# Kernel tuning notes

Measured on AMD Instinct MI355X. Metric: run time of the kernel, lower is better.

The kernel has to match this reference:

```python
import jax, jax.numpy as jnp
import numpy as np
from jax import lax

NFRAMES = 8
LAM = 0.1
SEQLEN, BS, DF = 25, 256, 16384  # 5-way 5-shot support, 256 queries, ResNet-50 feats per frame


def l2norm(x, eps=1e-12):
    return x / jnp.maximum(jnp.linalg.norm(x, axis=-1, keepdims=True), eps)


def dp(D, lam=LAM):
    """OTAM-style soft alignment DP.
    D: [B, n, n] frame cosine-similarity matrices.
    Returns [B] soft-max alignment scores (lam * logsumexp relaxation).
    Matches the torch code: DP[:,:,0]=D[:,:,0]; row 0 is a cumulative sum;
    DP[:,1:,i] = lam*logsumexp([DP[:,:-1,i-1], DP[:,1:,i-1]]/lam) + D[:,1:,i];
    result = lam*logsumexp(DP[:,:,-1]/lam).
    """
    col0 = D[:, :, 0]                       # [B, n]
    cols = jnp.moveaxis(D[:, :, 1:], 2, 0)  # [n-1, B, n] columns i=1..n-1

    def step(prev, d_col):
        # prev: DP column i-1, [B, n]; d_col: D column i, [B, n]
        two = jnp.stack([prev[:, :-1], prev[:, 1:]], axis=-1)      # [B, n-1, 2]
        lse = lam * jax.nn.logsumexp(two / lam, axis=-1)           # [B, n-1]
        row0 = prev[:, :1] + d_col[:, :1]                          # cumsum on row 0
        new = jnp.concatenate([row0, lse + d_col[:, 1:]], axis=1)  # [B, n]
        return new, None

    last, _ = lax.scan(step, col0, cols)    # last column of DP, [B, n]
    return lam * jax.nn.logsumexp(last / lam, axis=-1)             # [B]


def setup_inputs() -> dict:
    key = jax.random.key(0)
    k1, k2 = jax.random.split(key)
    support_vecs = jax.random.normal(k1, (SEQLEN, BS, DF), dtype=jnp.float32)
    target_vec = jax.random.normal(k2, (BS, DF), dtype=jnp.float32)
    return {"support_vecs": support_vecs, "target_vec": target_vec}


def reference(support_vecs, target_vec):
    seqlen, bs, df = support_vecs.shape
    n = NFRAMES
    sv = l2norm(support_vecs.reshape(seqlen, bs, n, -1))   # [S, B, n, f]
    tv = l2norm(target_vec.reshape(bs, n, -1))             # [B, n, f]
    # D[s,b,i,j] = <sv[s,b,i], tv[b,j]> : [S, B, n, n]
    D = jnp.einsum('sbif,bjf->sbij', sv, tv)
    Dflat = D.reshape(seqlen * bs, n, n)
    sim = 0.5 * (dp(Dflat) + dp(jnp.swapaxes(Dflat, 1, 2)))
    return sim.reshape(seqlen, bs)
```

## Files before the change

kernel.cpp:

```cpp
#include <hip/hip_runtime.h>
#include <hip/hip_bf16.h>


constexpr int kNF   = 8;
constexpr int kFLEN = 2048;
constexpr int kSeq  = 25;
constexpr int kBS   = 256;
constexpr int kDF   = 16384;
constexpr float kLam    = 0.1f;
constexpr float kInvLam = 10.0f;

__global__ __launch_bounds__(256, 2) void otam_kernel(
    const float* __restrict__ sv,
    const float* __restrict__ tv,
    float* __restrict__ out)
{
    __shared__ float V[kDF];
    __shared__ float sdot[kNF][kNF];
    __shared__ float snu[kNF];
    __shared__ float snv[kNF];
    __shared__ float sD[kNF][kNF];

    const int bid = blockIdx.x;
    const int s = bid % kSeq;
    const int b = bid / kSeq;
    const int t = threadIdx.x;

    {
        const float4* tv4 = (const float4*)(tv + (size_t)b * kDF);
        float4* V4 = (float4*)V;
        #pragma unroll
        for (int it = 0; it < 16; ++it)
            V4[it * 256 + t] = tv4[it * 256 + t];
    }
    __syncthreads();

    const int g = t >> 5;
    const int l = t & 31;

    float v2 = 0.f;
    {
        const float4* Vg = (const float4*)(V + g * kFLEN);
        #pragma unroll 4
        for (int c = 0; c < 16; ++c) {
            float4 v = Vg[c * 32 + l];
            v2 = fmaf(v.x, v.x, v2); v2 = fmaf(v.y, v.y, v2);
            v2 = fmaf(v.z, v.z, v2); v2 = fmaf(v.w, v.w, v2);
        }
    }

    float dot[kNF] = {};
    float u2 = 0.f;
    const float4* U4 = (const float4*)(sv + ((size_t)s * kBS + b) * kDF + (size_t)g * kFLEN);
    #pragma unroll 4
    for (int c = 0; c < 16; ++c) {
        float4 u = U4[c * 32 + l];
        u2 = fmaf(u.x, u.x, fmaf(u.y, u.y, fmaf(u.z, u.z, fmaf(u.w, u.w, u2))));
        #pragma unroll
        for (int j = 0; j < kNF; ++j) {
            float4 v = ((const float4*)(V + j * kFLEN))[c * 32 + l];
            dot[j] = fmaf(u.x, v.x, fmaf(u.y, v.y, fmaf(u.z, v.z, fmaf(u.w, v.w, dot[j]))));
        }
    }

    #pragma unroll
    for (int m = 16; m >= 1; m >>= 1) {
        u2 += __shfl_xor(u2, m, 64);
        v2 += __shfl_xor(v2, m, 64);
        #pragma unroll
        for (int j = 0; j < kNF; ++j) dot[j] += __shfl_xor(dot[j], m, 64);
    }
    if (l == 0) {
        snu[g] = u2;
        snv[g] = v2;
        #pragma unroll
        for (int j = 0; j < kNF; ++j) sdot[g][j] = dot[j];
    }
    __syncthreads();

    if (t < 64) {
        const int i = t >> 3, j = t & 7;
        sD[i][j] = sdot[i][j] * rsqrtf(snu[i]) * rsqrtf(snv[j]);
    }
    __syncthreads();

    if (t < 16) {
        const int r = t & 7;
        const bool xp = (t >= 8);

        auto Dm = [&](int rr, int ii) -> float {
            return xp ? sD[ii][rr] : sD[rr][ii];
        };

        float prev = Dm(r, 0);
        #pragma unroll
        for (int i = 1; i < kNF; ++i) {
            float up = __shfl_up(prev, 1, 64);
            float d  = Dm(r, i);
            float mx = fmaxf(up, prev);
            float mn = fminf(up, prev);
            float lse = mx + kLam * log1pf(expf((mn - mx) * kInvLam));
            prev = (r == 0) ? (prev + d) : (lse + d);
        }
        float mx = prev;
        #pragma unroll
        for (int m = 4; m >= 1; m >>= 1) mx = fmaxf(mx, __shfl_xor(mx, m, 64));
        float e = expf((prev - mx) * kInvLam);
        #pragma unroll
        for (int m = 4; m >= 1; m >>= 1) e += __shfl_xor(e, m, 64);
        float res = mx + kLam * logf(e);

        float resT = __shfl(res, (t & 7) + 8, 64);
        if (t == 0) out[(size_t)s * kBS + b] = 0.5f * (res + resT);
    }
}

extern "C" void kernel_launch(void* const* d_in, const int* in_sizes, int n_in,
                              void* d_out, int out_size, void* d_ws, size_t ws_size,
                              hipStream_t stream) {
    const float* sv = (const float*)d_in[0];
    const float* tv = (const float*)d_in[1];
    float* out = (float*)d_out;
    otam_kernel<<<dim3(kSeq * kBS), dim3(256), 0, stream>>>(sv, tv, out);
}
```

Measured before the change: 575.5 us.

## Reuse staged target features across many support sequences per block with register prefetch

```diff
diff --git a/kernel.cpp b/kernel.cpp
--- a/kernel.cpp
+++ b/kernel.cpp
@@ -1,5 +1,4 @@
 #include <hip/hip_runtime.h>
-#include <hip/hip_bf16.h>
 
 
 constexpr int kNF   = 8;
@@ -16,15 +15,21 @@
     float* __restrict__ out)
 {
     __shared__ float V[kDF];
-    __shared__ float sdot[kNF][kNF];
-    __shared__ float snu[kNF];
-    __shared__ float snv[kNF];
-    __shared__ float sD[kNF][kNF];
+    __shared__ float sdot[2][2][kNF][kNF];
+    __shared__ float rsnu[2][2][kNF];
+    __shared__ float rnv[kNF];
 
-    const int bid = blockIdx.x;
-    const int s = bid % kSeq;
-    const int b = bid / kSeq;
-    const int t = threadIdx.x;
+    const int bid  = blockIdx.x;
+    const int b    = bid >> 1;
+    const int half = bid & 1;
+    const int t    = threadIdx.x;
+    const int g    = t >> 5;
+    const int l    = t & 31;
+    const int lane = t & 63;
+
+    const int sbeg   = half ? 12 : 0;
+    const int scnt   = half ? 13 : 12;
+    const int npairs = (scnt + 1) >> 1;
 
     {
         const float4* tv4 = (const float4*)(tv + (size_t)b * kDF);
@@ -33,85 +38,114 @@
         for (int it = 0; it < 16; ++it)
             V4[it * 256 + t] = tv4[it * 256 + t];
     }
-    __syncthreads();
 
-    const int g = t >> 5;
-    const int l = t & 31;
-
-    float v2 = 0.f;
+    float4 u0[16], u1[16];
     {
-        const float4* Vg = (const float4*)(V + g * kFLEN);
-        #pragma unroll 4
-        for (int c = 0; c < 16; ++c) {
-            float4 v = Vg[c * 32 + l];
-            v2 = fmaf(v.x, v.x, v2); v2 = fmaf(v.y, v.y, v2);
-            v2 = fmaf(v.z, v.z, v2); v2 = fmaf(v.w, v.w, v2);
-        }
-    }
-
-    float dot[kNF] = {};
-    float u2 = 0.f;
-    const float4* U4 = (const float4*)(sv + ((size_t)s * kBS + b) * kDF + (size_t)g * kFLEN);
-    #pragma unroll 4
-    for (int c = 0; c < 16; ++c) {
-        float4 u = U4[c * 32 + l];
-        u2 = fmaf(u.x, u.x, fmaf(u.y, u.y, fmaf(u.z, u.z, fmaf(u.w, u.w, u2))));
+        const float4* p0 = (const float4*)(sv + ((size_t)(sbeg + 0) * kBS + b) * kDF + (size_t)g * kFLEN);
+        const float4* p1 = (const float4*)(sv + ((size_t)(sbeg + 1) * kBS + b) * kDF + (size_t)g * kFLEN);
         #pragma unroll
-        for (int j = 0; j < kNF; ++j) {
-            float4 v = ((const float4*)(V + j * kFLEN))[c * 32 + l];
-            dot[j] = fmaf(u.x, v.x, fmaf(u.y, v.y, fmaf(u.z, v.z, fmaf(u.w, v.w, dot[j]))));
-        }
-    }
-
-    #pragma unroll
-    for (int m = 16; m >= 1; m >>= 1) {
-        u2 += __shfl_xor(u2, m, 64);
-        v2 += __shfl_xor(v2, m, 64);
-        #pragma unroll
-        for (int j = 0; j < kNF; ++j) dot[j] += __shfl_xor(dot[j], m, 64);
-    }
-    if (l == 0) {
-        snu[g] = u2;
-        snv[g] = v2;
-        #pragma unroll
-        for (int j = 0; j < kNF; ++j) sdot[g][j] = dot[j];
+        for (int c = 0; c < 16; ++c) { u0[c] = p0[c * 32 + l]; u1[c] = p1[c * 32 + l]; }
     }
     __syncthreads();
 
-    if (t < 64) {
-        const int i = t >> 3, j = t & 7;
-        sD[i][j] = sdot[i][j] * rsqrtf(snu[i]) * rsqrtf(snv[j]);
+    {
+        float v2 = 0.f;
+        const float4* Vg = (const float4*)(V + g * kFLEN);
+        #pragma unroll
+        for (int c = 0; c < 16; ++c) {
+            float4 v = Vg[c * 32 + l];
+            v2 = fmaf(v.x, v.x, fmaf(v.y, v.y, fmaf(v.z, v.z, fmaf(v.w, v.w, v2))));
+        }
+        #pragma unroll
+        for (int m = 16; m >= 1; m >>= 1) v2 += __shfl_xor(v2, m, 64);
+        if (l == 0) rnv[g] = rsqrtf(v2);
     }
-    __syncthreads();
 
-    if (t < 16) {
-        const int r = t & 7;
-        const bool xp = (t >= 8);
+    for (int k = 0; k < npairs; ++k) {
+        const int  s0     = sbeg + 2 * k;
+        const bool valid1 = (2 * k + 1) < scnt;
+        const int  slot   = k & 1;
 
-        auto Dm = [&](int rr, int ii) -> float {
-            return xp ? sD[ii][rr] : sD[rr][ii];
-        };
+        float dot0[kNF] = {}, dot1[kNF] = {};
+        float n0 = 0.f, n1 = 0.f;
+        #pragma unroll
+        for (int c = 0; c < 16; ++c) {
+            float4 a = u0[c], e2 = u1[c];
+            n0 = fmaf(a.x, a.x, fmaf(a.y, a.y, fmaf(a.z, a.z, fmaf(a.w, a.w, n0))));
+            n1 = fmaf(e2.x, e2.x, fmaf(e2.y, e2.y, fmaf(e2.z, e2.z, fmaf(e2.w, e2.w, n1))));
+            #pragma unroll
+            for (int j = 0; j < kNF; ++j) {
+                float4 v = ((const float4*)(V + j * kFLEN))[c * 32 + l];
+                dot0[j] = fmaf(a.x, v.x, fmaf(a.y, v.y, fmaf(a.z, v.z, fmaf(a.w, v.w, dot0[j]))));
+                dot1[j] = fmaf(e2.x, v.x, fmaf(e2.y, v.y, fmaf(e2.z, v.z, fmaf(e2.w, v.w, dot1[j]))));
+            }
+        }
 
-        float prev = Dm(r, 0);
+        if (k + 1 < npairs) {
+            const int ns0 = s0 + 2;
+            const int ns1 = min(ns0 + 1, sbeg + scnt - 1);
+            const float4* p0 = (const float4*)(sv + ((size_t)ns0 * kBS + b) * kDF + (size_t)g * kFLEN);
+            const float4* p1 = (const float4*)(sv + ((size_t)ns1 * kBS + b) * kDF + (size_t)g * kFLEN);
+            #pragma unroll
+            for (int c = 0; c < 16; ++c) { u0[c] = p0[c * 32 + l]; u1[c] = p1[c * 32 + l]; }
+        }
+
         #pragma unroll
-        for (int i = 1; i < kNF; ++i) {
-            float up = __shfl_up(prev, 1, 64);
-            float d  = Dm(r, i);
-            float mx = fmaxf(up, prev);
-            float mn = fminf(up, prev);
-            float lse = mx + kLam * log1pf(expf((mn - mx) * kInvLam));
-            prev = (r == 0) ? (prev + d) : (lse + d);
+        for (int m = 16; m >= 1; m >>= 1) {
+            n0 += __shfl_xor(n0, m, 64);
+            n1 += __shfl_xor(n1, m, 64);
+            #pragma unroll
+            for (int j = 0; j < kNF; ++j) {
+                dot0[j] += __shfl_xor(dot0[j], m, 64);
+                dot1[j] += __shfl_xor(dot1[j], m, 64);
+            }
         }
-        float mx = prev;
-        #pragma unroll
-        for (int m = 4; m >= 1; m >>= 1) mx = fmaxf(mx, __shfl_xor(mx, m, 64));
-        float e = expf((prev - mx) * kInvLam);
-        #pragma unroll
-        for (int m = 4; m >= 1; m >>= 1) e += __shfl_xor(e, m, 64);
-        float res = mx + kLam * logf(e);
+        if (l == 0) {
+            rsnu[slot][0][g] = rsqrtf(n0);
+            rsnu[slot][1][g] = rsqrtf(n1);
+            #pragma unroll
+            for (int j = 0; j < kNF; ++j) {
+                sdot[slot][0][g][j] = dot0[j];
+                sdot[slot][1][g][j] = dot1[j];
+            }
+        }
+        __syncthreads();
 
-        float resT = __shfl(res, (t & 7) + 8, 64);
-        if (t == 0) out[(size_t)s * kBS + b] = 0.5f * (res + resT);
+        if ((t >> 6) == (k & 3) && lane < 32) {
+            const int  sub = lane >> 4;
+            const int  idx = lane & 15;
+            const int  r   = idx & 7;
+            const bool xp  = idx >= 8;
+            const float (*M)[kNF] = sdot[slot][sub];
+            const float* ru = rsnu[slot][sub];
+
+            auto Dm = [&](int rr, int ii) -> float {
+                return xp ? M[ii][rr] * ru[ii] * rnv[rr]
+                          : M[rr][ii] * ru[rr] * rnv[ii];
+            };
+
+            float prev = Dm(r, 0);
+            #pragma unroll
+            for (int i = 1; i < kNF; ++i) {
+                float up = __shfl_up(prev, 1, 64);
+                float d  = Dm(r, i);
+                float mx = fmaxf(up, prev);
+                float mn = fminf(up, prev);
+                float lse = mx + kLam * log1pf(expf((mn - mx) * kInvLam));
+                prev = (r == 0) ? (prev + d) : (lse + d);
+            }
+            float mx = prev;
+            #pragma unroll
+            for (int m = 4; m >= 1; m >>= 1) mx = fmaxf(mx, __shfl_xor(mx, m, 64));
+            float e = expf((prev - mx) * kInvLam);
+            #pragma unroll
+            for (int m = 4; m >= 1; m >>= 1) e += __shfl_xor(e, m, 64);
+            float res = mx + kLam * logf(e);
+
+            float resT = __shfl(res, lane + 8, 64);
+            if (idx == 0 && (sub == 0 || valid1))
+                out[(size_t)(s0 + sub) * kBS + b] = 0.5f * (res + resT);
+        }
     }
 }
 
@@ -121,5 +155,5 @@
     const float* sv = (const float*)d_in[0];
     const float* tv = (const float*)d_in[1];
     float* out = (float*)d_out;
-    otam_kernel<<<dim3(kSeq * kBS), dim3(256), 0, stream>>>(sv, tv, out);
+    otam_kernel<<<dim3(2 * kBS), dim3(256), 0, stream>>>(sv, tv, out);
 }
```

Result: slower. 1.404 ms (+143.9%).
